# Optimization experiments

Measured on AMD Instinct MI355X. Metric: run time of the kernel, lower is better.

## Reference

```python
import jax, jax.numpy as jnp
import numpy as np

N = 131072        # active input voxels (= output voxels for submanifold conv)
KVOL = 27         # 3x3x3 kernel volume
P = 65536         # neighbor pairs per kernel offset (regularized kernel map)
CIN = 64
COUT = 64


def setup_inputs() -> dict:
    key = jax.random.key(0)
    k1, k2, k3, k4, k5 = jax.random.split(key, 5)
    in_feats = jax.random.normal(k1, (N, CIN), dtype=jnp.float32)
    kernel = jax.random.normal(k2, (KVOL, CIN, COUT), dtype=jnp.float32) * (1.0 / np.sqrt(CIN * KVOL))
    bias_param = jax.random.normal(k3, (COUT,), dtype=jnp.float32)
    imap = jax.random.randint(k4, (KVOL, P), 0, N, dtype=jnp.int32)
    omap = jax.random.randint(k5, (KVOL, P), 0, N, dtype=jnp.int32)
    return {"in_feats": in_feats, "kernel": kernel, "bias_param": bias_param,
            "imap": imap, "omap": omap}


def reference(in_feats, kernel, bias_param, imap, omap):
    # Sparse 3D conv as gather -> per-offset GEMM -> scatter-add.
    # gathered: [KVOL, P, CIN]
    gathered = in_feats[imap]
    # per-offset GEMM: [KVOL, P, COUT]
    contrib = jnp.einsum('kpc,kco->kpo', gathered, kernel)
    out = jnp.zeros((N, COUT), dtype=in_feats.dtype)
    out = out.at[omap.reshape(-1)].add(contrib.reshape(-1, COUT))
    out = out + bias_param
    return out
```

## Files before the change

kernel.cpp:

```cpp
#include <hip/hip_runtime.h>
#include <hip/hip_bf16.h>
#include <stdint.h>

#define N_VOX 131072
#define KVOL  27
#define PPK   65536
#define CIN   64
#define COUT  64
#define TOT   (KVOL * PPK)
#define SORT_BLOCKS 864
#define GEMM_BLOCKS (KVOL * (PPK / 128))
#define NB    512

typedef __attribute__((ext_vector_type(8))) short short8;
typedef __attribute__((ext_vector_type(4))) float f32x4;

__device__ __forceinline__ void gl_lds16(const void* g, void* l) {
  __builtin_amdgcn_global_load_lds(
      (const __attribute__((address_space(1))) unsigned int*)g,
      (__attribute__((address_space(3))) unsigned int*)l,
      16, 0, 0);
}

__device__ __forceinline__ unsigned short f2bf(float f) {
  __hip_bfloat16 h = __float2bfloat16(f);
  return *reinterpret_cast<unsigned short*>(&h);
}


__global__ __launch_bounds__(256) void prep_hist_kernel(
    const float* __restrict__ in, unsigned short* __restrict__ inb,
    const float* __restrict__ w, unsigned short* __restrict__ wt,
    const int* __restrict__ omap, int* __restrict__ counts, int do_sort) {
  int b = blockIdx.x;
  if (do_sort) {
    if (b < SORT_BLOCKS) {
      __shared__ unsigned int hist[NB];
      int tid = threadIdx.x;
      hist[tid] = 0; hist[tid + 256] = 0;
      __syncthreads();
      int e0 = (b * 256 + tid) * 8;
      int4 o0 = *(const int4*)(omap + e0);
      int4 o1 = *(const int4*)(omap + e0 + 4);
      atomicAdd(&hist[(unsigned)o0.x >> 8], 1u);
      atomicAdd(&hist[(unsigned)o0.y >> 8], 1u);
      atomicAdd(&hist[(unsigned)o0.z >> 8], 1u);
      atomicAdd(&hist[(unsigned)o0.w >> 8], 1u);
      atomicAdd(&hist[(unsigned)o1.x >> 8], 1u);
      atomicAdd(&hist[(unsigned)o1.y >> 8], 1u);
      atomicAdd(&hist[(unsigned)o1.z >> 8], 1u);
      atomicAdd(&hist[(unsigned)o1.w >> 8], 1u);
      __syncthreads();
      counts[(size_t)b * NB + tid]       = (int)hist[tid];
      counts[(size_t)b * NB + tid + 256] = (int)hist[tid + 256];
      return;
    }
    b -= SORT_BLOCKS;
  }
  if (b < 4096) {
    int i = b * 256 + threadIdx.x;
    const float4* in4 = (const float4*)in;
    float4 f0 = in4[2 * i], f1 = in4[2 * i + 1];
    union { unsigned short u[8]; short8 v; } r;
    r.u[0] = f2bf(f0.x); r.u[1] = f2bf(f0.y); r.u[2] = f2bf(f0.z); r.u[3] = f2bf(f0.w);
    r.u[4] = f2bf(f1.x); r.u[5] = f2bf(f1.y); r.u[6] = f2bf(f1.z); r.u[7] = f2bf(f1.w);
    ((short8*)inb)[i] = r.v;
  } else {
    int k = b - 4096;
    const float* wk = w + k * CIN * COUT;
    unsigned short* wtk = wt + k * CIN * COUT;
    for (int idx = threadIdx.x; idx < CIN * COUT; idx += 256) {
      int c = idx >> 6, o = idx & 63;
      wtk[o * 64 + c] = f2bf(wk[idx]);
    }
  }
}


__global__ __launch_bounds__(256) void scan_blocks_kernel(
    const int* __restrict__ counts, int* __restrict__ blockbase,
    int* __restrict__ totals) {
  __shared__ int s[256];
  int b = blockIdx.x, t = threadIdx.x;
  int c0 = 0, c1 = 0, c2 = 0, c3 = 0;
  if (t < 216) {
    c0 = counts[(size_t)(4 * t + 0) * NB + b];
    c1 = counts[(size_t)(4 * t + 1) * NB + b];
    c2 = counts[(size_t)(4 * t + 2) * NB + b];
    c3 = counts[(size_t)(4 * t + 3) * NB + b];
  }
  int sum = c0 + c1 + c2 + c3;
  s[t] = sum; __syncthreads();
  for (int off = 1; off < 256; off <<= 1) {
    int v = (t >= off) ? s[t - off] : 0;
    __syncthreads();
    s[t] += v;
    __syncthreads();
  }
  int excl = s[t] - sum;
  int* brow = blockbase + (size_t)b * SORT_BLOCKS;
  if (t < 216) {
    brow[t * 4]     = excl;
    brow[t * 4 + 1] = excl + c0;
    brow[t * 4 + 2] = excl + c0 + c1;
    brow[t * 4 + 3] = excl + c0 + c1 + c2;
  }
  if (t == 255) totals[b] = s[255];
}


__global__ __launch_bounds__(NB) void base_kernel(const int* __restrict__ totals,
                                                  int* __restrict__ bbase) {
  __shared__ int s[NB];
  int t = threadIdx.x;
  int v = totals[t];
  s[t] = v; __syncthreads();
  for (int off = 1; off < NB; off <<= 1) {
    int x = (t >= off) ? s[t - off] : 0;
    __syncthreads();
    s[t] += x;
    __syncthreads();
  }
  bbase[t] = s[t] - v;
  if (t == NB - 1) bbase[NB] = s[NB - 1];
}


__global__ __launch_bounds__(256) void scatter_kernel(
    const int* __restrict__ omap, const int* __restrict__ blockbase,
    const int* __restrict__ bbase, int* __restrict__ islot,
    unsigned char* __restrict__ lokey) {
  __shared__ unsigned int gb[NB];
  __shared__ unsigned int cur[NB];
  int b = blockIdx.x, tid = threadIdx.x;
  for (int i = tid; i < NB; i += 256) {
    gb[i] = (unsigned)(bbase[i] + blockbase[(size_t)i * SORT_BLOCKS + b]);
    cur[i] = 0;
  }
  __syncthreads();
  int e0 = (b * 256 + tid) * 8;
  int4 o0 = *(const int4*)(omap + e0);
  int4 o1 = *(const int4*)(omap + e0 + 4);
  unsigned int key[8] = {(unsigned)o0.x, (unsigned)o0.y, (unsigned)o0.z, (unsigned)o0.w,
                         (unsigned)o1.x, (unsigned)o1.y, (unsigned)o1.z, (unsigned)o1.w};
  int res[8];
#pragma unroll
  for (int i = 0; i < 8; i++) {
    unsigned int bk = key[i] >> 8;
    unsigned int r = atomicAdd(&cur[bk], 1u);
    unsigned int pos = gb[bk] + r;
    res[i] = (int)(pos << 8) | (int)(key[i] & 255u);
    lokey[pos] = (unsigned char)(key[i] & 255u);
  }
  *(int4*)(islot + e0)     = make_int4(res[0], res[1], res[2], res[3]);
  *(int4*)(islot + e0 + 4) = make_int4(res[4], res[5], res[6], res[7]);
}


__global__ __launch_bounds__(256) void refine_kernel(
    const unsigned char* __restrict__ lokey,
    const int* __restrict__ bbase,
    int* __restrict__ fmap, int* __restrict__ ofs, int* __restrict__ cnt) {
  __shared__ unsigned int hist[256];
  __shared__ unsigned int scn[256];
  __shared__ unsigned int cur[256];
  int b = blockIdx.x, t = threadIdx.x;
  int sb = bbase[b], se = bbase[b + 1], n = se - sb;
  hist[t] = 0;
  __syncthreads();
  for (int i = t; i < n; i += 256)
    atomicAdd(&hist[lokey[sb + i]], 1u);
  __syncthreads();
  unsigned int h = hist[t];
  scn[t] = h;
  __syncthreads();
  for (int off = 1; off < 256; off <<= 1) {
    unsigned int v = (t >= off) ? scn[t - off] : 0;
    __syncthreads();
    scn[t] += v;
    __syncthreads();
  }
  unsigned int excl = scn[t] - h;
  ofs[b * 256 + t] = sb + (int)excl;
  cnt[b * 256 + t] = (int)h;
  cur[t] = excl;
  __syncthreads();
  for (int i = t; i < n; i += 256) {
    unsigned int lo = lokey[sb + i];
    unsigned int r = atomicAdd(&cur[lo], 1u);
    fmap[sb + i] = sb + (int)r;
  }
}


__global__ __launch_bounds__(256) void spconv_store_kernel(
    const unsigned short* __restrict__ inb,
    const unsigned short* __restrict__ wt,
    const int* __restrict__ imap,
    const int* __restrict__ islot,
    const int* __restrict__ fmap,
    unsigned short* __restrict__ contrib) {
  __shared__ __align__(16) char smem[24576];
  short* A_lds = (short*)smem;
  short* B_lds = (short*)(smem + 16384);
  short* C_sh  = (short*)smem;
  __shared__ int perm_s[128];

  int bid = blockIdx.x;
  int k = bid >> 9;
  int pbase = (bid & 511) * 128;
  int tid = threadIdx.x;
  int wave = tid >> 6, lane = tid & 63;
  int m = lane & 15, q = lane >> 4;

  const int* imk = imap + k * PPK;
  const unsigned short* wtk = wt + k * 4096;

  if (tid < 128)
    perm_s[tid] = fmap[((unsigned)islot[k * PPK + pbase + tid]) >> 8];

#pragma unroll
  for (int i = 0; i < 2; i++) {
    int id = wave * 2 + i;
    int t = id >> 1, s = id & 1;
    const unsigned short* g = wtk + (t * 16 + m) * 64 + s * 32 + q * 8;
    gl_lds16(g, &B_lds[(t * 128 + s * 64) * 8]);
  }
#pragma unroll
  for (int j = 0; j < 2; j++) {
    int r = wave * 2 + j;
    int row = imk[pbase + r * 16 + m];
    const unsigned short* g0 = inb + row * 64 + q * 8;
    gl_lds16(g0,      &A_lds[(r * 128)      * 8]);
    gl_lds16(g0 + 32, &A_lds[(r * 128 + 64) * 8]);
  }
  __syncthreads();

  const short8* Af = (const short8*)A_lds;
  const short8* Bf = (const short8*)B_lds;

  short8 a[2][2], b[4][2];
#pragma unroll
  for (int r2 = 0; r2 < 2; r2++) {
    int r = wave * 2 + r2;
#pragma unroll
    for (int s = 0; s < 2; s++) a[r2][s] = Af[r * 128 + s * 64 + lane];
  }
#pragma unroll
  for (int t = 0; t < 4; t++)
#pragma unroll
    for (int s = 0; s < 2; s++) b[t][s] = Bf[t * 128 + s * 64 + lane];

  __syncthreads();

  f32x4 acc[2][4];
#pragma unroll
  for (int r2 = 0; r2 < 2; r2++)
#pragma unroll
    for (int t = 0; t < 4; t++) {
      f32x4 c = {0.f, 0.f, 0.f, 0.f};
      c = __builtin_amdgcn_mfma_f32_16x16x32_bf16(a[r2][0], b[t][0], c, 0, 0, 0);
      c = __builtin_amdgcn_mfma_f32_16x16x32_bf16(a[r2][1], b[t][1], c, 0, 0, 0);
      acc[r2][t] = c;
    }

#pragma unroll
  for (int r2 = 0; r2 < 2; r2++) {
    int pl = (wave * 2 + r2) * 16 + q * 4;
#pragma unroll
    for (int t = 0; t < 4; t++)
#pragma unroll
      for (int reg = 0; reg < 4; reg++)
        C_sh[(pl + reg) * 72 + t * 16 + m] = (short)f2bf(acc[r2][t][reg]);
  }
  __syncthreads();

#pragma unroll
  for (int i = 0; i < 4; i++) {
    int id = i * 256 + tid;
    int row = id >> 3, ch = (id & 7) * 8;
    short8 v = *(const short8*)&C_sh[row * 72 + ch];
    __builtin_nontemporal_store(v, (short8*)&contrib[(size_t)perm_s[row] * 64 + ch]);
  }
}


__global__ __launch_bounds__(256) void reduce_kernel(
    const unsigned short* __restrict__ contrib,
    const int* __restrict__ ofs,
    const int* __restrict__ cnt,
    const float* __restrict__ bias,
    float* __restrict__ out) {
  int row = blockIdx.x * 4 + (threadIdx.x >> 6);
  int lane = threadIdx.x & 63;
  int rg = lane >> 3, ch = (lane & 7) * 8;
  int s = ofs[row], n = cnt[row];

  float acc[8];
#pragma unroll
  for (int i = 0; i < 8; i++) acc[i] = 0.f;

  int j = rg;
  for (; j + 8 < n; j += 16) {
    short8 v0 = __builtin_nontemporal_load((const short8*)&contrib[(size_t)(s + j) * 64 + ch]);
    short8 v1 = __builtin_nontemporal_load((const short8*)&contrib[(size_t)(s + j + 8) * 64 + ch]);
#pragma unroll
    for (int i = 0; i < 8; i++)
      acc[i] += __uint_as_float((unsigned int)(unsigned short)v0[i] << 16);
#pragma unroll
    for (int i = 0; i < 8; i++)
      acc[i] += __uint_as_float((unsigned int)(unsigned short)v1[i] << 16);
  }
  if (j < n) {
    short8 v0 = __builtin_nontemporal_load((const short8*)&contrib[(size_t)(s + j) * 64 + ch]);
#pragma unroll
    for (int i = 0; i < 8; i++)
      acc[i] += __uint_as_float((unsigned int)(unsigned short)v0[i] << 16);
  }

#pragma unroll
  for (int mask = 8; mask < 64; mask <<= 1)
#pragma unroll
    for (int i = 0; i < 8; i++) acc[i] += __shfl_xor(acc[i], mask, 64);

  if (rg == 0) {
    float4 b0 = *(const float4*)(bias + ch);
    float4 b1 = *(const float4*)(bias + ch + 4);
    float4 r0 = {acc[0] + b0.x, acc[1] + b0.y, acc[2] + b0.z, acc[3] + b0.w};
    float4 r1 = {acc[4] + b1.x, acc[5] + b1.y, acc[6] + b1.z, acc[7] + b1.w};
    *(float4*)(out + (size_t)row * 64 + ch) = r0;
    *(float4*)(out + (size_t)row * 64 + ch + 4) = r1;
  }
}


__global__ __launch_bounds__(256) void init_out_kernel(float* __restrict__ out,
                                                       const float* __restrict__ bias) {
  int i = blockIdx.x * blockDim.x + threadIdx.x;
  float4 b = *(const float4*)(bias + ((i * 4) & 63));
  ((float4*)out)[i] = b;
}

__global__ __launch_bounds__(256) void spconv_atomic_kernel(
    const unsigned short* __restrict__ inb,
    const unsigned short* __restrict__ wt,
    const int* __restrict__ imap, const int* __restrict__ omap,
    float* __restrict__ out) {
  __shared__ __align__(16) short A_lds[128 * 64];
  __shared__ __align__(16) short B_lds[64 * 64];

  int bid = blockIdx.x;
  int k = bid >> 9;
  int pbase = (bid & 511) * 128;
  int tid = threadIdx.x;
  int wave = tid >> 6, lane = tid & 63;
  int m = lane & 15, q = lane >> 4;

  const int* imk = imap + k * PPK;
  const int* omk = omap + k * PPK;
  const unsigned short* wtk = wt + k * 4096;

#pragma unroll
  for (int i = 0; i < 2; i++) {
    int id = wave * 2 + i;
    int t = id >> 1, s = id & 1;
    const unsigned short* g = wtk + (t * 16 + m) * 64 + s * 32 + q * 8;
    gl_lds16(g, &B_lds[(t * 128 + s * 64) * 8]);
  }
#pragma unroll
  for (int j = 0; j < 2; j++) {
    int r = wave * 2 + j;
    int row = imk[pbase + r * 16 + m];
    const unsigned short* g0 = inb + row * 64 + q * 8;
    gl_lds16(g0,      &A_lds[(r * 128)      * 8]);
    gl_lds16(g0 + 32, &A_lds[(r * 128 + 64) * 8]);
  }
  __syncthreads();

  const short8* Af = (const short8*)A_lds;
  const short8* Bf = (const short8*)B_lds;
  short8 a[2][2], b[4][2];
#pragma unroll
  for (int r2 = 0; r2 < 2; r2++) {
    int r = wave * 2 + r2;
#pragma unroll
    for (int s = 0; s < 2; s++) a[r2][s] = Af[r * 128 + s * 64 + lane];
  }
#pragma unroll
  for (int t = 0; t < 4; t++)
#pragma unroll
    for (int s = 0; s < 2; s++) b[t][s] = Bf[t * 128 + s * 64 + lane];

  f32x4 acc[2][4];
#pragma unroll
  for (int r2 = 0; r2 < 2; r2++)
#pragma unroll
    for (int t = 0; t < 4; t++) {
      f32x4 c = {0.f, 0.f, 0.f, 0.f};
      c = __builtin_amdgcn_mfma_f32_16x16x32_bf16(a[r2][0], b[t][0], c, 0, 0, 0);
      c = __builtin_amdgcn_mfma_f32_16x16x32_bf16(a[r2][1], b[t][1], c, 0, 0, 0);
      acc[r2][t] = c;
    }

  int orow[2][4];
#pragma unroll
  for (int r2 = 0; r2 < 2; r2++) {
    int pr = pbase + (wave * 2 + r2) * 16 + q * 4;
#pragma unroll
    for (int reg = 0; reg < 4; reg++) orow[r2][reg] = omk[pr + reg];
  }
#pragma unroll
  for (int r2 = 0; r2 < 2; r2++)
#pragma unroll
    for (int t = 0; t < 4; t++)
#pragma unroll
      for (int reg = 0; reg < 4; reg++)
        atomicAdd(out + (size_t)orow[r2][reg] * 64 + t * 16 + m, acc[r2][t][reg]);
}


extern "C" void kernel_launch(void* const* d_in, const int* in_sizes, int n_in,
                              void* d_out, int out_size, void* d_ws, size_t ws_size,
                              hipStream_t stream) {
  const float* in_feats = (const float*)d_in[0];
  const float* kern     = (const float*)d_in[1];
  const float* bias     = (const float*)d_in[2];
  const int*   imap     = (const int*)d_in[3];
  const int*   omap     = (const int*)d_in[4];
  float* out = (float*)d_out;

  char* ws = (char*)d_ws;
  size_t off = 0;
  auto alloc = [&](size_t bytes) { size_t o = off; off = (off + bytes + 255) & ~(size_t)255; return o; };

  size_t o_inb   = alloc((size_t)N_VOX * CIN * 2);
  size_t o_wt    = alloc((size_t)KVOL * CIN * COUT * 2);
  size_t o_cts   = alloc((size_t)NB * SORT_BLOCKS * 4);
  size_t o_bb    = alloc((size_t)NB * SORT_BLOCKS * 4);
  size_t o_tot   = alloc((size_t)NB * 4);
  size_t o_bbase = alloc((size_t)(NB + 1) * 4);
  size_t o_islot = alloc((size_t)TOT * 4);
  size_t o_lok   = alloc((size_t)TOT);
  size_t o_fmap  = alloc((size_t)TOT * 4);
  size_t o_ctb   = alloc((size_t)TOT * 64 * 2);
  size_t needed = off;

  unsigned short* inb = (unsigned short*)(ws + o_inb);
  unsigned short* wt  = (unsigned short*)(ws + o_wt);
  int* counts    = (int*)(ws + o_cts);
  int* blockbase = (int*)(ws + o_bb);
  int* totals    = (int*)(ws + o_tot);
  int* bbase     = (int*)(ws + o_bbase);
  int* islot     = (int*)(ws + o_islot);
  unsigned char* lokey = (unsigned char*)(ws + o_lok);
  int* fmap      = (int*)(ws + o_fmap);
  unsigned short* ctb  = (unsigned short*)(ws + o_ctb);
  int* ofs = (int*)(ws + o_cts);
  int* cnt = ofs + N_VOX;

  bool fast = (ws_size >= needed);

  if (fast) {
    prep_hist_kernel<<<SORT_BLOCKS + 4096 + KVOL, 256, 0, stream>>>(
        in_feats, inb, kern, wt, omap, counts, 1);
    scan_blocks_kernel<<<NB, 256, 0, stream>>>(counts, blockbase, totals);
    base_kernel<<<1, NB, 0, stream>>>(totals, bbase);
    scatter_kernel<<<SORT_BLOCKS, 256, 0, stream>>>(omap, blockbase, bbase, islot, lokey);
    refine_kernel<<<NB, 256, 0, stream>>>(lokey, bbase, fmap, ofs, cnt);
    spconv_store_kernel<<<GEMM_BLOCKS, 256, 0, stream>>>(inb, wt, imap, islot, fmap, ctb);
    reduce_kernel<<<N_VOX / 4, 256, 0, stream>>>(ctb, ofs, cnt, bias, out);
  } else {
    prep_hist_kernel<<<4096 + KVOL, 256, 0, stream>>>(
        in_feats, inb, kern, wt, omap, nullptr, 0);
    init_out_kernel<<<(N_VOX * COUT / 4) / 256, 256, 0, stream>>>(out, bias);
    spconv_atomic_kernel<<<GEMM_BLOCKS, 256, 0, stream>>>(inb, wt, imap, omap, out);
  }
}
```

Measured before the change: 263.9 us.

## Fold base scan into scatter/refine and emit direct slot map via packed pairs

Removes the single-block base_kernel launch by having scatter and refine redundantly scan the 512 bucket totals in shared memory. Scatter now writes packed (element index, low key) pairs into the contrib buffer region instead of separate islot and lokey arrays. Refine then writes the final sorted slot for each element directly, so the GEMM kernel needs one read instead of a two-level islot->fmap lookup. The reduce kernel also switches from nontemporal loads to ordinary loads. The trade-offs are refine's scattered 4-byte writes and the repeated scan work in every block.

New measurement: 279.9 us. +6.1%, slower.

```diff
diff --git a/kernel.cpp b/kernel.cpp
--- a/kernel.cpp
+++ b/kernel.cpp
@@ -14,6 +14,15 @@
 
 typedef __attribute__((ext_vector_type(8))) short short8;
 typedef __attribute__((ext_vector_type(4))) float f32x4;
+
+#define SCAN512(s, tid)                                       \
+  for (int off = 1; off < 512; off <<= 1) {                   \
+    int va_ = ((tid) >= off) ? s[(tid) - off] : 0;            \
+    int vb_ = (((tid) + 256) >= off) ? s[(tid) + 256 - off] : 0; \
+    __syncthreads();                                          \
+    s[(tid)] += va_; s[(tid) + 256] += vb_;                   \
+    __syncthreads();                                          \
+  }
 
 __device__ __forceinline__ void gl_lds16(const void* g, void* l) {
   __builtin_amdgcn_global_load_lds(
@@ -109,67 +118,58 @@
 }
 
 
-__global__ __launch_bounds__(NB) void base_kernel(const int* __restrict__ totals,
-                                                  int* __restrict__ bbase) {
-  __shared__ int s[NB];
-  int t = threadIdx.x;
-  int v = totals[t];
-  s[t] = v; __syncthreads();
-  for (int off = 1; off < NB; off <<= 1) {
-    int x = (t >= off) ? s[t - off] : 0;
-    __syncthreads();
-    s[t] += x;
-    __syncthreads();
-  }
-  bbase[t] = s[t] - v;
-  if (t == NB - 1) bbase[NB] = s[NB - 1];
-}
-
-
 __global__ __launch_bounds__(256) void scatter_kernel(
     const int* __restrict__ omap, const int* __restrict__ blockbase,
-    const int* __restrict__ bbase, int* __restrict__ islot,
-    unsigned char* __restrict__ lokey) {
+    const int* __restrict__ totals, unsigned int* __restrict__ pairs) {
+  __shared__ int ts[NB];
   __shared__ unsigned int gb[NB];
   __shared__ unsigned int cur[NB];
   int b = blockIdx.x, tid = threadIdx.x;
-  for (int i = tid; i < NB; i += 256) {
-    gb[i] = (unsigned)(bbase[i] + blockbase[(size_t)i * SORT_BLOCKS + b]);
-    cur[i] = 0;
-  }
+  int t0 = totals[tid], t1 = totals[tid + 256];
+  ts[tid] = t0; ts[tid + 256] = t1;
+  __syncthreads();
+  SCAN512(ts, tid);
+  gb[tid]       = (unsigned)(ts[tid] - t0 +
+                    blockbase[(size_t)tid * SORT_BLOCKS + b]);
+  gb[tid + 256] = (unsigned)(ts[tid + 256] - t1 +
+                    blockbase[(size_t)(tid + 256) * SORT_BLOCKS + b]);
+  cur[tid] = 0; cur[tid + 256] = 0;
   __syncthreads();
   int e0 = (b * 256 + tid) * 8;
   int4 o0 = *(const int4*)(omap + e0);
   int4 o1 = *(const int4*)(omap + e0 + 4);
   unsigned int key[8] = {(unsigned)o0.x, (unsigned)o0.y, (unsigned)o0.z, (unsigned)o0.w,
                          (unsigned)o1.x, (unsigned)o1.y, (unsigned)o1.z, (unsigned)o1.w};
-  int res[8];
 #pragma unroll
   for (int i = 0; i < 8; i++) {
     unsigned int bk = key[i] >> 8;
     unsigned int r = atomicAdd(&cur[bk], 1u);
     unsigned int pos = gb[bk] + r;
-    res[i] = (int)(pos << 8) | (int)(key[i] & 255u);
-    lokey[pos] = (unsigned char)(key[i] & 255u);
-  }
-  *(int4*)(islot + e0)     = make_int4(res[0], res[1], res[2], res[3]);
-  *(int4*)(islot + e0 + 4) = make_int4(res[4], res[5], res[6], res[7]);
+    pairs[pos] = (((unsigned)(e0 + i)) << 8) | (key[i] & 255u);
+  }
 }
 
 
 __global__ __launch_bounds__(256) void refine_kernel(
-    const unsigned char* __restrict__ lokey,
-    const int* __restrict__ bbase,
-    int* __restrict__ fmap, int* __restrict__ ofs, int* __restrict__ cnt) {
+    const unsigned int* __restrict__ pairs, const int* __restrict__ totals,
+    int* __restrict__ islotf, int* __restrict__ ofs, int* __restrict__ cnt) {
+  __shared__ int ts[NB];
   __shared__ unsigned int hist[256];
   __shared__ unsigned int scn[256];
   __shared__ unsigned int cur[256];
   int b = blockIdx.x, t = threadIdx.x;
-  int sb = bbase[b], se = bbase[b + 1], n = se - sb;
+  int t0 = totals[t], t1 = totals[t + 256];
+  ts[t] = t0; ts[t + 256] = t1;
   hist[t] = 0;
   __syncthreads();
+  SCAN512(ts, t);
+  __shared__ int sb_s, n_s;
+  if (t == 0) { n_s = totals[b]; sb_s = ts[b] - n_s; }
+  __syncthreads();
+  int sb = sb_s, n = n_s;
+
   for (int i = t; i < n; i += 256)
-    atomicAdd(&hist[lokey[sb + i]], 1u);
+    atomicAdd(&hist[pairs[sb + i] & 255u], 1u);
   __syncthreads();
   unsigned int h = hist[t];
   scn[t] = h;
@@ -186,9 +186,9 @@
   cur[t] = excl;
   __syncthreads();
   for (int i = t; i < n; i += 256) {
-    unsigned int lo = lokey[sb + i];
-    unsigned int r = atomicAdd(&cur[lo], 1u);
-    fmap[sb + i] = sb + (int)r;
+    unsigned int v = pairs[sb + i];
+    unsigned int r = atomicAdd(&cur[v & 255u], 1u);
+    islotf[v >> 8] = sb + (int)r;
   }
 }
 
@@ -197,8 +197,7 @@
     const unsigned short* __restrict__ inb,
     const unsigned short* __restrict__ wt,
     const int* __restrict__ imap,
-    const int* __restrict__ islot,
-    const int* __restrict__ fmap,
+    const int* __restrict__ islotf,
     unsigned short* __restrict__ contrib) {
   __shared__ __align__(16) char smem[24576];
   short* A_lds = (short*)smem;
@@ -216,8 +215,7 @@
   const int* imk = imap + k * PPK;
   const unsigned short* wtk = wt + k * 4096;
 
-  if (tid < 128)
-    perm_s[tid] = fmap[((unsigned)islot[k * PPK + pbase + tid]) >> 8];
+  if (tid < 128) perm_s[tid] = islotf[k * PPK + pbase + tid];
 
 #pragma unroll
   for (int i = 0; i < 2; i++) {
@@ -302,8 +300,8 @@
 
   int j = rg;
   for (; j + 8 < n; j += 16) {
-    short8 v0 = __builtin_nontemporal_load((const short8*)&contrib[(size_t)(s + j) * 64 + ch]);
-    short8 v1 = __builtin_nontemporal_load((const short8*)&contrib[(size_t)(s + j + 8) * 64 + ch]);
+    short8 v0 = *((const short8*)&contrib[(size_t)(s + j) * 64 + ch]);
+    short8 v1 = *((const short8*)&contrib[(size_t)(s + j + 8) * 64 + ch]);
 #pragma unroll
     for (int i = 0; i < 8; i++)
       acc[i] += __uint_as_float((unsigned int)(unsigned short)v0[i] << 16);
@@ -312,7 +310,7 @@
       acc[i] += __uint_as_float((unsigned int)(unsigned short)v1[i] << 16);
   }
   if (j < n) {
-    short8 v0 = __builtin_nontemporal_load((const short8*)&contrib[(size_t)(s + j) * 64 + ch]);
+    short8 v0 = *((const short8*)&contrib[(size_t)(s + j) * 64 + ch]);
 #pragma unroll
     for (int i = 0; i < 8; i++)
       acc[i] += __uint_as_float((unsigned int)(unsigned short)v0[i] << 16);
@@ -438,10 +436,7 @@
   size_t o_cts   = alloc((size_t)NB * SORT_BLOCKS * 4);
   size_t o_bb    = alloc((size_t)NB * SORT_BLOCKS * 4);
   size_t o_tot   = alloc((size_t)NB * 4);
-  size_t o_bbase = alloc((size_t)(NB + 1) * 4);
   size_t o_islot = alloc((size_t)TOT * 4);
-  size_t o_lok   = alloc((size_t)TOT);
-  size_t o_fmap  = alloc((size_t)TOT * 4);
   size_t o_ctb   = alloc((size_t)TOT * 64 * 2);
   size_t needed = off;
 
@@ -450,11 +445,9 @@
   int* counts    = (int*)(ws + o_cts);
   int* blockbase = (int*)(ws + o_bb);
   int* totals    = (int*)(ws + o_tot);
-  int* bbase     = (int*)(ws + o_bbase);
-  int* islot     = (int*)(ws + o_islot);
-  unsigned char* lokey = (unsigned char*)(ws + o_lok);
-  int* fmap      = (int*)(ws + o_fmap);
-  unsigned short* ctb  = (unsigned short*)(ws + o_ctb);
+  int* islotf    = (int*)(ws + o_islot);
+  unsigned short* ctb = (unsigned short*)(ws + o_ctb);
+  unsigned int* pairs = (unsigned int*)(ws + o_ctb);
   int* ofs = (int*)(ws + o_cts);
   int* cnt = ofs + N_VOX;
 
@@ -464,10 +457,9 @@
     prep_hist_kernel<<<SORT_BLOCKS + 4096 + KVOL, 256, 0, stream>>>(
         in_feats, inb, kern, wt, omap, counts, 1);
     scan_blocks_kernel<<<NB, 256, 0, stream>>>(counts, blockbase, totals);
-    base_kernel<<<1, NB, 0, stream>>>(totals, bbase);
-    scatter_kernel<<<SORT_BLOCKS, 256, 0, stream>>>(omap, blockbase, bbase, islot, lokey);
-    refine_kernel<<<NB, 256, 0, stream>>>(lokey, bbase, fmap, ofs, cnt);
-    spconv_store_kernel<<<GEMM_BLOCKS, 256, 0, stream>>>(inb, wt, imap, islot, fmap, ctb);
+    scatter_kernel<<<SORT_BLOCKS, 256, 0, stream>>>(omap, blockbase, totals, pairs);
+    refine_kernel<<<NB, 256, 0, stream>>>(pairs, totals, islotf, ofs, cnt);
+    spconv_store_kernel<<<GEMM_BLOCKS, 256, 0, stream>>>(inb, wt, imap, islotf, ctb);
     reduce_kernel<<<N_VOX / 4, 256, 0, stream>>>(ctb, ofs, cnt, bias, out);
   } else {
     prep_hist_kernel<<<4096 + KVOL, 256, 0, stream>>>(
```
